# Optimization experiments

Hardware: AMD Instinct MI355X
Metric: run time of the kernel (lower is better)

Reference implementation:

```python
import jax, jax.numpy as jnp
import numpy as np
from jax.scipy.special import logsumexp

EPS_OT = 0.05      # self.eps in AttentionOT
MAX_ITER = 100     # Sinkhorn max_iter (torch early-stops; at convergence results match)


def _l2norm(x):
    # F.normalize(x, dim=-1, p=2) with eps=1e-12
    return x / jnp.maximum(jnp.linalg.norm(x, axis=-1, keepdims=True), 1e-12)


def _sinkhorn(Cmat, mu, nu, eps):
    # Cmat: (BK, M, N), mu: (BK, M), nu: (BK, N)
    log_mu = jnp.log(mu + 1e-8)
    log_nu = jnp.log(nu + 1e-8)

    def kern(u, v):
        # log Boltzmann kernel: (-C + u_i + v_j) / eps, shape (BK, M, N)
        return (-Cmat + u[..., :, None] + v[..., None, :]) / eps

    def step(carry, _):
        u, v = carry
        u = eps * (log_mu - logsumexp(kern(u, v), axis=2)) + u
        v = eps * (log_nu - logsumexp(kern(u, v), axis=1)) + v
        return (u, v), None

    u0 = jnp.zeros_like(mu)
    v0 = jnp.zeros_like(nu)
    (u, v), _ = jax.lax.scan(jax.checkpoint(step), (u0, v0), None, length=MAX_ITER)
    return jnp.exp(kern(u, v))  # transport plan T, (BK, M, N)


def setup_inputs() -> dict:
    key = jax.random.key(0)
    Nq, M, B, K, C = 64, 16, 8, 256, 512
    ks = jax.random.split(key, 8)
    s = 1.0 / np.sqrt(C)  # torch nn.Linear default init bound
    return {
        "xq": jax.random.normal(ks[0], (Nq, M, B, C), jnp.float32),
        "xk": jax.random.normal(ks[1], (B, K, C), jnp.float32),
        "xv": jax.random.normal(ks[2], (B, K, C), jnp.float32),
        "Wq": jax.random.uniform(ks[3], (C, C), jnp.float32, -s, s),
        "Wk": jax.random.uniform(ks[4], (C, C), jnp.float32, -s, s),
        "Wv": jax.random.uniform(ks[5], (C, C), jnp.float32, -s, s),
        "Wp": jax.random.uniform(ks[6], (C, C), jnp.float32, -s, s),
        "bp": jax.random.uniform(ks[7], (C,), jnp.float32, -s, s),
    }


def reference(xq, xk, xv, Wq, Wk, Wv, Wp, bp):
    Nq, M, B, C = xq.shape
    K = xk.shape[1]
    # projections (qkv_bias=False; proj has bias). dropout probs are 0 -> identity.
    q = _l2norm(xq @ Wq.T)          # (Nq, M, B, C)
    kk = _l2norm(xk @ Wk.T)         # (B, K, C)
    v = xv @ Wv.T                   # (B, K, C)
    # torch: einsum('bkc,nmbc->bnkm') then permute(0,2,3,1) -> (B,K,M,Nq)
    sim = jnp.einsum('bkc,nmbc->bkmn', kk, q).reshape(B * K, M, Nq)
    wdist = 1.0 - sim
    mu = jnp.full((B * K, M), 1.0 / M, dtype=sim.dtype)
    nu = jnp.full((B * K, Nq), 1.0 / Nq, dtype=sim.dtype)
    T = _sinkhorn(wdist, mu, nu, EPS_OT)            # (B*K, M, Nq)
    score_map = (M * Nq * sim * T).reshape(B, K, M, Nq)
    attn = T.reshape(B, K, M, Nq).transpose(3, 0, 1, 2)  # (Nq, B, K, M)
    x = jnp.einsum('nbkm,bkc->nmbc', attn, v)            # (Nq, M, B, C)
    x = x @ Wp.T + bp
    return x, score_map
```

## Files before the change

### kernel.cpp

```cpp
#include <hip/hip_runtime.h>


typedef short   short8  __attribute__((ext_vector_type(8)));
typedef float   floatx4 __attribute__((ext_vector_type(4)));
typedef unsigned int uint2e __attribute__((ext_vector_type(2)));

static __device__ __forceinline__ float fastrcp(float x) {
    return __builtin_amdgcn_rcpf(x);
}
static __device__ __forceinline__ unsigned short f2bf(float f) {
    union { float f; unsigned u; } c; c.f = f;
    unsigned r = c.u + 0x7FFF + ((c.u >> 16) & 1);
    return (unsigned short)(r >> 16);
}
static __device__ __forceinline__ float bf2f(unsigned short h) {
    union { unsigned u; float f; } c; c.u = (unsigned)h << 16;
    return c.f;
}

#if __has_builtin(__builtin_amdgcn_permlane16_swap)
static __device__ __forceinline__ float xadd16(float s) {
    uint2e r = __builtin_amdgcn_permlane16_swap(
        __float_as_uint(s), __float_as_uint(s), false, false);
    return __uint_as_float(r.x) + __uint_as_float(r.y);
}
#else
static __device__ __forceinline__ float xadd16(float s) {
    return s + __shfl_xor(s, 16, 64);
}
#endif
#if __has_builtin(__builtin_amdgcn_permlane32_swap)
static __device__ __forceinline__ float xadd32(float s) {
    uint2e r = __builtin_amdgcn_permlane32_swap(
        __float_as_uint(s), __float_as_uint(s), false, false);
    return __uint_as_float(r.x) + __uint_as_float(r.y);
}
#else
static __device__ __forceinline__ float xadd32(float s) {
    return s + __shfl_xor(s, 32, 64);
}
#endif

#define RRI(x, C) __builtin_amdgcn_update_dpp(0, (x), (C), 0xf, 0xf, true)
#define RRF(x, C) __int_as_float(RRI(__float_as_int(x), (C)))
#define GATH16(d, s) do { d[0] = (s);                                        \
    d[1]  = RRF((s), 0x121); d[2]  = RRF((s), 0x122);                        \
    d[3]  = RRF((s), 0x123); d[4]  = RRF((s), 0x124);                        \
    d[5]  = RRF((s), 0x125); d[6]  = RRF((s), 0x126);                        \
    d[7]  = RRF((s), 0x127); d[8]  = RRF((s), 0x128);                        \
    d[9]  = RRF((s), 0x129); d[10] = RRF((s), 0x12a);                        \
    d[11] = RRF((s), 0x12b); d[12] = RRF((s), 0x12c);                        \
    d[13] = RRF((s), 0x12d); d[14] = RRF((s), 0x12e);                        \
    d[15] = RRF((s), 0x12f); } while (0)

__global__ __launch_bounds__(256) void prep(
    const float* __restrict__ xq, const float* __restrict__ xk,
    const float* __restrict__ xv, const float* __restrict__ Wq,
    const float* __restrict__ Wk, const float* __restrict__ Wv,
    const float* __restrict__ Wp,
    unsigned short* __restrict__ xqh, unsigned short* __restrict__ xql,
    unsigned short* __restrict__ xkh, unsigned short* __restrict__ xkl,
    unsigned short* __restrict__ xvb,
    unsigned short* __restrict__ wqh, unsigned short* __restrict__ wql,
    unsigned short* __restrict__ wkh, unsigned short* __restrict__ wkl,
    unsigned short* __restrict__ wvb, unsigned short* __restrict__ wpb)
{
    const int b = blockIdx.x;
    const float* src; unsigned short *dh, *dl; long base;
    if (b < 4096)      { src = xq; dh = xqh; dl = xql;     base = (long)b * 256; }
    else if (b < 5120) { src = xk; dh = xkh; dl = xkl;     base = (long)(b - 4096) * 256; }
    else if (b < 6144) { src = xv; dh = xvb; dl = nullptr; base = (long)(b - 5120) * 256; }
    else if (b < 6400) { src = Wq; dh = wqh; dl = wql;     base = (long)(b - 6144) * 256; }
    else if (b < 6656) { src = Wk; dh = wkh; dl = wkl;     base = (long)(b - 6400) * 256; }
    else if (b < 6912) { src = Wv; dh = wvb; dl = nullptr; base = (long)(b - 6656) * 256; }
    else               { src = Wp; dh = wpb; dl = nullptr; base = (long)(b - 6912) * 256; }
    const long i = base + threadIdx.x;
    float4 v = ((const float4*)src)[i];
    ushort4 h;
    h.x = f2bf(v.x); h.y = f2bf(v.y); h.z = f2bf(v.z); h.w = f2bf(v.w);
    ((ushort4*)dh)[i] = h;
    if (dl) {
        ushort4 l;
        l.x = f2bf(v.x - bf2f(h.x)); l.y = f2bf(v.y - bf2f(h.y));
        l.z = f2bf(v.z - bf2f(h.z)); l.w = f2bf(v.w - bf2f(h.w));
        ((ushort4*)dl)[i] = l;
    }
}

__global__ __launch_bounds__(256, 3) void gemm_qkv2(
    const unsigned short* __restrict__ xqh, const unsigned short* __restrict__ xql,
    const unsigned short* __restrict__ xkh, const unsigned short* __restrict__ xkl,
    const unsigned short* __restrict__ xvb,
    const unsigned short* __restrict__ wqh, const unsigned short* __restrict__ wql,
    const unsigned short* __restrict__ wkh, const unsigned short* __restrict__ wkl,
    const unsigned short* __restrict__ wvb,
    unsigned short* __restrict__ qh, unsigned short* __restrict__ ql,
    unsigned short* __restrict__ kh, unsigned short* __restrict__ kl,
    unsigned short* __restrict__ vt)
{
    __shared__ __align__(16) short LB[15360];
    short (*Ash)[40] = (short(*)[40])(LB);
    short (*Asl)[40] = (short(*)[40])(LB + 2560);
    short (*Bsh)[40] = (short(*)[40])(LB + 5120);
    short (*Bsl)[40] = (short(*)[40])(LB + 10240);

    const int bt = blockIdx.y;
    const unsigned short *Ah, *Al, *Bh, *Bl;
    int seg, arow0;
    if (bt < 128)      { Ah = xqh; Al = xql; Bh = wqh; Bl = wql; arow0 = bt * 64;         seg = 0; }
    else if (bt < 160) { Ah = xkh; Al = xkl; Bh = wkh; Bl = wkl; arow0 = (bt - 128) * 64; seg = 1; }
    else               { Ah = xvb; Al = xvb; Bh = wvb; Bl = wvb; arow0 = (bt - 160) * 64; seg = 2; }
    const bool split = (seg != 2);

    const int tid  = threadIdx.x;
    const int lane = tid & 63, wv = tid >> 6;
    const int wc = wv * 32;
    const int j0 = blockIdx.x * 128;

    floatx4 acc[4][2];
#pragma unroll
    for (int i = 0; i < 4; i++)
#pragma unroll
        for (int j = 0; j < 2; j++) acc[i][j] = {0.f, 0.f, 0.f, 0.f};

    const int sr = tid >> 2, sch = (tid & 3) * 8;
    const int fr = lane & 15, fq = (lane >> 4) * 8;

    for (int k0 = 0; k0 < 512; k0 += 32) {
        {
            const long ao = (long)(arow0 + sr) * 512 + k0 + sch;
            *(short8*)&Ash[sr][sch] = *(const short8*)(Ah + ao);
            if (split) *(short8*)&Asl[sr][sch] = *(const short8*)(Al + ao);
        }
#pragma unroll
        for (int p = 0; p < 2; p++) {
            const int r = sr + p * 64;
            const long bo = (long)(j0 + r) * 512 + k0 + sch;
            *(short8*)&Bsh[r][sch] = *(const short8*)(Bh + bo);
            if (split) *(short8*)&Bsl[r][sch] = *(const short8*)(Bl + bo);
        }
        __syncthreads();
        short8 ah[4], bh[2];
#pragma unroll
        for (int i = 0; i < 4; i++) ah[i] = *(const short8*)&Ash[i * 16 + fr][fq];
#pragma unroll
        for (int j = 0; j < 2; j++) bh[j] = *(const short8*)&Bsh[wc + j * 16 + fr][fq];
        if (split) {
            short8 al[4], bl[2];
#pragma unroll
            for (int i = 0; i < 4; i++) al[i] = *(const short8*)&Asl[i * 16 + fr][fq];
#pragma unroll
            for (int j = 0; j < 2; j++) bl[j] = *(const short8*)&Bsl[wc + j * 16 + fr][fq];
#pragma unroll
            for (int i = 0; i < 4; i++)
#pragma unroll
                for (int j = 0; j < 2; j++) {
                    acc[i][j] = __builtin_amdgcn_mfma_f32_16x16x32_bf16(ah[i], bh[j], acc[i][j], 0, 0, 0);
                    acc[i][j] = __builtin_amdgcn_mfma_f32_16x16x32_bf16(ah[i], bl[j], acc[i][j], 0, 0, 0);
                    acc[i][j] = __builtin_amdgcn_mfma_f32_16x16x32_bf16(al[i], bh[j], acc[i][j], 0, 0, 0);
                }
        } else {
#pragma unroll
            for (int i = 0; i < 4; i++)
#pragma unroll
                for (int j = 0; j < 2; j++)
                    acc[i][j] = __builtin_amdgcn_mfma_f32_16x16x32_bf16(ah[i], bh[j], acc[i][j], 0, 0, 0);
        }
        __syncthreads();
    }

    const int cr = (lane >> 4) * 4, cc = lane & 15;
    if (seg == 2) {
        short (*S2)[72] = (short(*)[72])LB;
#pragma unroll
        for (int i = 0; i < 4; i++)
#pragma unroll
            for (int j = 0; j < 2; j++)
#pragma unroll
                for (int r = 0; r < 4; r++)
                    S2[wc + j * 16 + cc][i * 16 + cr + r] =
                        (short)f2bf(acc[i][j][r]);
        __syncthreads();
        const int orow = tid >> 1;
        const int os   = (tid & 1) * 32;
        unsigned short* dst = vt + (long)(arow0 >> 8) * 131072
                            + (long)(j0 + orow) * 256 + (arow0 & 255) + os;
#pragma unroll
        for (int c8 = 0; c8 < 4; c8++)
            *(short8*)(dst + c8 * 8) = *(const short8*)&S2[orow][os + c8 * 8];
    } else {
#pragma unroll
        for (int i = 0; i < 4; i++)
#pragma unroll
            for (int j = 0; j < 2; j++) {
                const int gj = j0 + wc + j * 16 + cc;
#pragma unroll
                for (int r = 0; r < 4; r++) {
                    const int gi = arow0 + i * 16 + cr + r;
                    const float v = acc[i][j][r];
                    const unsigned short h = f2bf(v);
                    const unsigned short lo = f2bf(v - bf2f(h));
                    if (seg == 0) {
                        const long orow = (long)((gi & 7) * 1024 + ((gi >> 3) & 15) * 64 + (gi >> 7));
                        qh[orow * 512 + gj] = h;
                        ql[orow * 512 + gj] = lo;
                    } else {
                        kh[(long)gi * 512 + gj] = h;
                        kl[(long)gi * 512 + gj] = lo;
                    }
                }
            }
    }
}

__global__ __launch_bounds__(256) void gemm_sim64(
    const short* __restrict__ Ah, const short* __restrict__ Al,
    const short* __restrict__ Bh, const short* __restrict__ Bl,
    float* __restrict__ Out, const float* __restrict__ rs)
{
    const int z = blockIdx.z;
    Ah += (long)z * 131072;  Al += (long)z * 131072;
    Bh += (long)z * 524288;  Bl += (long)z * 524288;
    Out += (long)z * 262144;
    const float* rsq = rs + (long)z * 1024;
    const float* rsk = rs + 8192 + (long)z * 256;

    __shared__ __align__(16) short Ash[64][40];
    __shared__ __align__(16) short Asl[64][40];
    __shared__ __align__(16) short Bsh[64][40];
    __shared__ __align__(16) short Bsl[64][40];

    const int tid  = threadIdx.x;
    const int lane = tid & 63, wv = tid >> 6;
    const int wr = (wv >> 1) * 32, wc = (wv & 1) * 32;
    const int i0 = blockIdx.x * 64, j0 = blockIdx.y * 64;

    floatx4 acc[2][2];
#pragma unroll
    for (int i = 0; i < 2; i++)
#pragma unroll
        for (int j = 0; j < 2; j++) acc[i][j] = {0.f, 0.f, 0.f, 0.f};

    const int sr = tid >> 2, sch = (tid & 3) * 8;
    const int fr = lane & 15, fq = (lane >> 4) * 8;

    for (int k0 = 0; k0 < 512; k0 += 32) {
        const long ao = (long)(i0 + sr) * 512 + k0 + sch;
        const long bo = (long)(j0 + sr) * 512 + k0 + sch;
        *(short8*)&Ash[sr][sch] = *(const short8*)(Ah + ao);
        *(short8*)&Asl[sr][sch] = *(const short8*)(Al + ao);
        *(short8*)&Bsh[sr][sch] = *(const short8*)(Bh + bo);
        *(short8*)&Bsl[sr][sch] = *(const short8*)(Bl + bo);
        __syncthreads();
        short8 ah[2], al[2], bh[2], bl[2];
#pragma unroll
        for (int i = 0; i < 2; i++) {
            ah[i] = *(const short8*)&Ash[wr + i * 16 + fr][fq];
            al[i] = *(const short8*)&Asl[wr + i * 16 + fr][fq];
        }
#pragma unroll
        for (int j = 0; j < 2; j++) {
            bh[j] = *(const short8*)&Bsh[wc + j * 16 + fr][fq];
            bl[j] = *(const short8*)&Bsl[wc + j * 16 + fr][fq];
        }
#pragma unroll
        for (int i = 0; i < 2; i++)
#pragma unroll
            for (int j = 0; j < 2; j++) {
                acc[i][j] = __builtin_amdgcn_mfma_f32_16x16x32_bf16(ah[i], bh[j], acc[i][j], 0, 0, 0);
                acc[i][j] = __builtin_amdgcn_mfma_f32_16x16x32_bf16(ah[i], bl[j], acc[i][j], 0, 0, 0);
                acc[i][j] = __builtin_amdgcn_mfma_f32_16x16x32_bf16(al[i], bh[j], acc[i][j], 0, 0, 0);
            }
        __syncthreads();
    }

    const int cr = (lane >> 4) * 4, cc = lane & 15;
#pragma unroll
    for (int i = 0; i < 2; i++)
#pragma unroll
        for (int j = 0; j < 2; j++) {
            const int gj = j0 + wc + j * 16 + cc;
            const float sq = rsq[gj];
#pragma unroll
            for (int r = 0; r < 4; r++) {
                const int gi = i0 + wr + i * 16 + cr + r;
                Out[(long)gi * 1024 + gj] = acc[i][j][r] * rsk[gi] * sq;
            }
        }
}

template <bool BIAS, bool OPERM, bool OUT_BF16>
__global__ __launch_bounds__(256) void gemm_bf16(
    const short* __restrict__ A, const short* __restrict__ B,
    const float* __restrict__ bias, void* __restrict__ OutV,
    int Kdim, int lda, int ldb, int ldo, long sA, long sB, long sO)
{
    __shared__ __align__(16) short As[128][40];
    __shared__ __align__(16) short Bs[128][40];

    const int tid  = threadIdx.x;
    const int lane = tid & 63, wv = tid >> 6;
    const int wr = (wv >> 1) * 64, wc = (wv & 1) * 64;
    const int i0 = blockIdx.x * 128, j0 = blockIdx.y * 128;

    floatx4 acc[4][4];
#pragma unroll
    for (int i = 0; i < 4; i++)
#pragma unroll
        for (int j = 0; j < 4; j++) acc[i][j] = {0.f, 0.f, 0.f, 0.f};

    const int sr = tid >> 2, sk = (tid & 3) * 8;
    const int fr = lane & 15, fq = (lane >> 4) * 8;
    const short* pa = A + (long)blockIdx.z * sA;
    const short* pb = B + (long)blockIdx.z * sB;

    for (int k0 = 0; k0 < Kdim; k0 += 32) {
#pragma unroll
        for (int p = 0; p < 2; p++) {
            *(short8*)&As[sr + p * 64][sk] =
                *(const short8*)(pa + (long)(i0 + sr + p * 64) * lda + k0 + sk);
            *(short8*)&Bs[sr + p * 64][sk] =
                *(const short8*)(pb + (long)(j0 + sr + p * 64) * ldb + k0 + sk);
        }
        __syncthreads();
        short8 af[4], bf[4];
#pragma unroll
        for (int i = 0; i < 4; i++) af[i] = *(const short8*)&As[wr + i * 16 + fr][fq];
#pragma unroll
        for (int j = 0; j < 4; j++) bf[j] = *(const short8*)&Bs[wc + j * 16 + fr][fq];
#pragma unroll
        for (int i = 0; i < 4; i++)
#pragma unroll
            for (int j = 0; j < 4; j++)
                acc[i][j] = __builtin_amdgcn_mfma_f32_16x16x32_bf16(af[i], bf[j], acc[i][j], 0, 0, 0);
        __syncthreads();
    }

    float* Of = nullptr; unsigned short* Ob = nullptr;
    if constexpr (OUT_BF16) Ob = (unsigned short*)OutV + (long)blockIdx.z * sO;
    else                    Of = (float*)OutV + (long)blockIdx.z * sO;
    const int cr = (lane >> 4) * 4, cc = lane & 15;
#pragma unroll
    for (int i = 0; i < 4; i++) {
#pragma unroll
        for (int j = 0; j < 4; j++) {
            const int gj = j0 + wc + j * 16 + cc;
            float bb = 0.0f;
            if constexpr (BIAS) bb = bias[gj];
#pragma unroll
            for (int r = 0; r < 4; r++) {
                const int gi = i0 + wr + i * 16 + cr + r;
                float v = acc[i][j][r] + bb;
                long idx;
                if constexpr (OPERM)
                    idx = (long)((gi & 63) * 128 + ((gi >> 6) & 15) * 8 + (gi >> 10)) * ldo + gj;
                else
                    idx = (long)gi * ldo + gj;
                if constexpr (OUT_BF16) Ob[idx] = f2bf(v);
                else                    Of[idx] = v;
            }
        }
    }
}

__global__ __launch_bounds__(256) void rownorm(
    const unsigned short* __restrict__ qh, const unsigned short* __restrict__ ql,
    const unsigned short* __restrict__ kh, const unsigned short* __restrict__ kl,
    float* __restrict__ rs)
{
    const int row  = blockIdx.x * 4 + (threadIdx.x >> 6);
    const int lane = threadIdx.x & 63;
    const unsigned short *ph, *pl;
    long r;
    if (row < 8192) { ph = qh; pl = ql; r = row; }
    else            { ph = kh; pl = kl; r = row - 8192; }
    const long o = r * 512 + lane * 8;
    ushort4 h0 = *(const ushort4*)(ph + o), h1 = *(const ushort4*)(ph + o + 4);
    ushort4 l0 = *(const ushort4*)(pl + o), l1 = *(const ushort4*)(pl + o + 4);
    float ss = 0.0f;
    const unsigned short hv[8] = {h0.x, h0.y, h0.z, h0.w, h1.x, h1.y, h1.z, h1.w};
    const unsigned short lv[8] = {l0.x, l0.y, l0.z, l0.w, l1.x, l1.y, l1.z, l1.w};
#pragma unroll
    for (int i = 0; i < 8; i++) {
        const float v = bf2f(hv[i]) + bf2f(lv[i]);
        ss = fmaf(v, v, ss);
    }
#pragma unroll
    for (int off = 32; off; off >>= 1) ss += __shfl_xor(ss, off, 64);
    if (lane == 0) rs[row] = 1.0f / fmaxf(sqrtf(ss), 1e-12f);
}

__global__ __launch_bounds__(256, 2) void sinkhorn5(
    const float* __restrict__ sim, float* __restrict__ score,
    unsigned short* __restrict__ Tt)
{
    const int lane = threadIdx.x & 63;
    const int bk   = blockIdx.x * 4 + (threadIdx.x >> 6);
    const float* S = sim + (long)bk * 1024;
    const int m = lane & 15, g = lane >> 4;

    int idx[16];
    idx[0] = m;
    idx[1]  = RRI(m, 0x121); idx[2]  = RRI(m, 0x122); idx[3]  = RRI(m, 0x123);
    idx[4]  = RRI(m, 0x124); idx[5]  = RRI(m, 0x125); idx[6]  = RRI(m, 0x126);
    idx[7]  = RRI(m, 0x127); idx[8]  = RRI(m, 0x128); idx[9]  = RRI(m, 0x129);
    idx[10] = RRI(m, 0x12a); idx[11] = RRI(m, 0x12b); idx[12] = RRI(m, 0x12c);
    idx[13] = RRI(m, 0x12d); idx[14] = RRI(m, 0x12e); idx[15] = RRI(m, 0x12f);

    float K1[16], K2R[16], sv[16];
#pragma unroll
    for (int j = 0; j < 16; j++) {
        K1[j] = __expf((S[m * 64 + g * 16 + idx[j]] - 1.0f) * 20.0f);
        const float s_ = S[idx[j] * 64 + lane];
        sv[j]  = s_;
        K2R[j] = __expf((s_ - 1.0f) * 20.0f);
    }

    const float muP = 0.0625f + 1e-8f;
    const float nuP = 0.015625f + 1e-8f;
    float b = 1.0f;
    float aB[16], bB[16];
#pragma unroll
    for (int j = 0; j < 16; j++) bB[j] = 1.0f;

#pragma unroll 1
    for (int it = 0; it < 100; it++) {
        float s0 = 0, s1 = 0, s2 = 0, s3 = 0;
#pragma unroll
        for (int j = 0; j < 4; j++) {
            s0 = fmaf(K1[j],      bB[j],      s0);
            s1 = fmaf(K1[4 + j],  bB[4 + j],  s1);
            s2 = fmaf(K1[8 + j],  bB[8 + j],  s2);
            s3 = fmaf(K1[12 + j], bB[12 + j], s3);
        }
        float s = (s0 + s1) + (s2 + s3);
        s = xadd16(s);
        s = xadd32(s);
        const float a = muP * fastrcp(s);
        GATH16(aB, a);
        float t0 = 0, t1 = 0, t2 = 0, t3 = 0;
#pragma unroll
        for (int j = 0; j < 4; j++) {
            t0 = fmaf(K2R[j],      aB[j],      t0);
            t1 = fmaf(K2R[4 + j],  aB[4 + j],  t1);
            t2 = fmaf(K2R[8 + j],  aB[8 + j],  t2);
            t3 = fmaf(K2R[12 + j], aB[12 + j], t3);
        }
        const float bp_ = b;
        b = nuP * fastrcp((t0 + t1) + (t2 + t3));
        GATH16(bB, b);
        const int conv = __builtin_fabsf(b - bp_) <= 1e-5f * __builtin_fabsf(b);
        if (__all(conv)) break;
    }

    float* Sc = score + (long)bk * 1024;
    unsigned short* Tp = Tt + (long)(bk >> 8) * 262144 + (bk & 255);
#pragma unroll
    for (int j = 0; j < 16; j++) {
        const int row = idx[j];
        const float Tv = aB[j] * K2R[j] * b;
        Sc[row * 64 + lane] = 1024.0f * sv[j] * Tv;
        Tp[(long)(row * 64 + lane) * 256] = f2bf(Tv);
    }
}

extern "C" void kernel_launch(void* const* d_in, const int* in_sizes, int n_in,
                              void* d_out, int out_size, void* d_ws, size_t ws_size,
                              hipStream_t stream)
{
    (void)in_sizes; (void)n_in; (void)out_size; (void)ws_size;
    const float* xq = (const float*)d_in[0];
    const float* xk = (const float*)d_in[1];
    const float* xv = (const float*)d_in[2];
    const float* Wq = (const float*)d_in[3];
    const float* Wk = (const float*)d_in[4];
    const float* Wv = (const float*)d_in[5];
    const float* Wp = (const float*)d_in[6];
    const float* bp = (const float*)d_in[7];

    float* out_x     = (float*)d_out;
    float* out_score = out_x + 8192L * 512;

    char* W = (char*)d_ws;
    const long MB = 1 << 20;
    unsigned short* qh   = (unsigned short*)(W + 0);
    unsigned short* ql   = (unsigned short*)(W + 8 * MB);
    unsigned short* xq_h = (unsigned short*)(W + 16 * MB);
    float*          simb = (float*)(W + 16 * MB);
    unsigned short* xq_l = (unsigned short*)(W + 24 * MB);
    unsigned short* xpre = (unsigned short*)(W + 24 * MB);
    unsigned short* xk_h = (unsigned short*)(W + 32 * MB);
    unsigned short* xk_l = (unsigned short*)(W + 34 * MB);
    unsigned short* Tt   = (unsigned short*)(W + 32 * MB);
    unsigned short* xv_b = (unsigned short*)(W + 36 * MB);
    unsigned short* kh   = (unsigned short*)(W + 38 * MB);
    unsigned short* kl   = (unsigned short*)(W + 40 * MB);
    unsigned short* vt   = (unsigned short*)(W + 42 * MB);
    unsigned short* wqh  = (unsigned short*)(W + 44 * MB);
    unsigned short* wql  = (unsigned short*)(W + 44 * MB + 1 * 524288);
    unsigned short* wkh  = (unsigned short*)(W + 44 * MB + 2 * 524288);
    unsigned short* wkl  = (unsigned short*)(W + 44 * MB + 3 * 524288);
    unsigned short* wvb  = (unsigned short*)(W + 44 * MB + 4 * 524288);
    unsigned short* wpb  = (unsigned short*)(W + 44 * MB + 5 * 524288);
    float*          rs   = (float*)(W + 47 * MB);

    const dim3 blk(256);

    prep<<<7168, blk, 0, stream>>>(xq, xk, xv, Wq, Wk, Wv, Wp,
                                   xq_h, xq_l, xk_h, xk_l, xv_b,
                                   wqh, wql, wkh, wkl, wvb, wpb);

    gemm_qkv2<<<dim3(4, 192), blk, 0, stream>>>(
        xq_h, xq_l, xk_h, xk_l, xv_b, wqh, wql, wkh, wkl, wvb,
        qh, ql, kh, kl, vt);

    rownorm<<<2560, blk, 0, stream>>>(qh, ql, kh, kl, rs);

    gemm_sim64<<<dim3(4, 16, 8), blk, 0, stream>>>(
        (const short*)kh, (const short*)kl, (const short*)qh, (const short*)ql,
        simb, rs);

    sinkhorn5<<<512, blk, 0, stream>>>(simb, out_score, Tt);

    gemm_bf16<false, false, true><<<dim3(8, 4, 8), blk, 0, stream>>>(
        (const short*)Tt, (const short*)vt, nullptr, xpre,
        256, 256, 256, 512, 262144, 131072, 524288);

    gemm_bf16<true, true, false><<<dim3(64, 4), blk, 0, stream>>>(
        (const short*)xpre, (const short*)wpb, bp, out_x,
        512, 512, 512, 512, 0, 0, 0);
}
```

Baseline: 200.1 us.

## Double-buffer QKV GEMM with direct-to-LDS loads and fuse row norms into sim GEMM

The QKV projection GEMM now loads tiles with global_load_lds straight into a double-buffered LDS area, prefetching the next K-slice while the current one runs on MFMA. Its grid is transposed so consecutive blocks share the same weight column tile. The separate rownorm kernel is removed; gemm_sim64 now accumulates the squared norms of its q and k rows from the tiles it already loads and applies the normalisation in its epilogue. This drops one launch and a reread of q and k, at the cost of more LDS in the QKV kernel, which may lower its occupancy, and a few extra FMAs per element in the sim GEMM.

```diff
diff --git a/kernel.cpp b/kernel.cpp
--- a/kernel.cpp
+++ b/kernel.cpp
@@ -16,6 +16,12 @@
 static __device__ __forceinline__ float bf2f(unsigned short h) {
     union { unsigned u; float f; } c; c.u = (unsigned)h << 16;
     return c.f;
+}
+
+static __device__ __forceinline__ void gll16(const unsigned short* g, short* l) {
+    __builtin_amdgcn_global_load_lds(
+        (const __attribute__((address_space(1))) void*)g,
+        (__attribute__((address_space(3))) void*)l, 16, 0, 0);
 }
 
 #if __has_builtin(__builtin_amdgcn_permlane16_swap)
@@ -98,13 +104,9 @@
     unsigned short* __restrict__ kh, unsigned short* __restrict__ kl,
     unsigned short* __restrict__ vt)
 {
-    __shared__ __align__(16) short LB[15360];
-    short (*Ash)[40] = (short(*)[40])(LB);
-    short (*Asl)[40] = (short(*)[40])(LB + 2560);
-    short (*Bsh)[40] = (short(*)[40])(LB + 5120);
-    short (*Bsl)[40] = (short(*)[40])(LB + 10240);
-
-    const int bt = blockIdx.y;
+    __shared__ __align__(16) short LB[24576];
+
+    const int bt = blockIdx.x;
     const unsigned short *Ah, *Al, *Bh, *Bl;
     int seg, arow0;
     if (bt < 128)      { Ah = xqh; Al = xql; Bh = wqh; Bl = wql; arow0 = bt * 64;         seg = 0; }
@@ -115,7 +117,7 @@
     const int tid  = threadIdx.x;
     const int lane = tid & 63, wv = tid >> 6;
     const int wc = wv * 32;
-    const int j0 = blockIdx.x * 128;
+    const int j0 = blockIdx.y * 128;
 
     floatx4 acc[4][2];
 #pragma unroll
@@ -123,34 +125,50 @@
 #pragma unroll
         for (int j = 0; j < 2; j++) acc[i][j] = {0.f, 0.f, 0.f, 0.f};
 
-    const int sr = tid >> 2, sch = (tid & 3) * 8;
+    const int lrow = lane >> 2;
+    const int lch  = (lane & 3) * 8;
+    const int gra  = 16 * wv;
+    const int grb  = 32 * wv;
+    const long gA0 = (long)(arow0 + gra + lrow) * 512 + lch;
+    const long gB0 = (long)(j0    + grb + lrow) * 512 + lch;
+
     const int fr = lane & 15, fq = (lane >> 4) * 8;
 
-    for (int k0 = 0; k0 < 512; k0 += 32) {
-        {
-            const long ao = (long)(arow0 + sr) * 512 + k0 + sch;
-            *(short8*)&Ash[sr][sch] = *(const short8*)(Ah + ao);
-            if (split) *(short8*)&Asl[sr][sch] = *(const short8*)(Al + ao);
-        }
-#pragma unroll
-        for (int p = 0; p < 2; p++) {
-            const int r = sr + p * 64;
-            const long bo = (long)(j0 + r) * 512 + k0 + sch;
-            *(short8*)&Bsh[r][sch] = *(const short8*)(Bh + bo);
-            if (split) *(short8*)&Bsl[r][sch] = *(const short8*)(Bl + bo);
-        }
-        __syncthreads();
+#define QKV_STAGE(d, k0) do {                                                 \
+        short* bb = LB + (d) * 12288;                                         \
+        gll16(Ah + gA0 + (k0),            bb + gra * 32);                     \
+        gll16(Bh + gB0 + (k0),            bb + 4096 + grb * 32);              \
+        gll16(Bh + gB0 + (k0) + 16 * 512, bb + 4096 + (grb + 16) * 32);       \
+        if (split) {                                                          \
+            gll16(Al + gA0 + (k0),            bb + 2048 + gra * 32);          \
+            gll16(Bl + gB0 + (k0),            bb + 8192 + grb * 32);          \
+            gll16(Bl + gB0 + (k0) + 16 * 512, bb + 8192 + (grb + 16) * 32);   \
+        }                                                                     \
+    } while (0)
+
+    QKV_STAGE(0, 0);
+    __syncthreads();
+
+#pragma unroll 2
+    for (int t = 0; t < 16; t++) {
+        const int cur = t & 1;
+        if (t < 15) QKV_STAGE(cur ^ 1, (t + 1) * 32);
+        const short* base = LB + cur * 12288;
         short8 ah[4], bh[2];
 #pragma unroll
-        for (int i = 0; i < 4; i++) ah[i] = *(const short8*)&Ash[i * 16 + fr][fq];
-#pragma unroll
-        for (int j = 0; j < 2; j++) bh[j] = *(const short8*)&Bsh[wc + j * 16 + fr][fq];
+        for (int i = 0; i < 4; i++)
+            ah[i] = *(const short8*)&base[(i * 16 + fr) * 32 + fq];
+#pragma unroll
+        for (int j = 0; j < 2; j++)
+            bh[j] = *(const short8*)&base[4096 + (wc + j * 16 + fr) * 32 + fq];
         if (split) {
             short8 al[4], bl[2];
 #pragma unroll
-            for (int i = 0; i < 4; i++) al[i] = *(const short8*)&Asl[i * 16 + fr][fq];
-#pragma unroll
-            for (int j = 0; j < 2; j++) bl[j] = *(const short8*)&Bsl[wc + j * 16 + fr][fq];
+            for (int i = 0; i < 4; i++)
+                al[i] = *(const short8*)&base[2048 + (i * 16 + fr) * 32 + fq];
+#pragma unroll
+            for (int j = 0; j < 2; j++)
+                bl[j] = *(const short8*)&base[8192 + (wc + j * 16 + fr) * 32 + fq];
 #pragma unroll
             for (int i = 0; i < 4; i++)
 #pragma unroll
@@ -168,6 +186,7 @@
         }
         __syncthreads();
     }
+#undef QKV_STAGE
 
     const int cr = (lane >> 4) * 4, cc = lane & 15;
     if (seg == 2) {
@@ -216,19 +235,19 @@
 __global__ __launch_bounds__(256) void gemm_sim64(
     const short* __restrict__ Ah, const short* __restrict__ Al,
     const short* __restrict__ Bh, const short* __restrict__ Bl,
-    float* __restrict__ Out, const float* __restrict__ rs)
+    float* __restrict__ Out)
 {
     const int z = blockIdx.z;
     Ah += (long)z * 131072;  Al += (long)z * 131072;
     Bh += (long)z * 524288;  Bl += (long)z * 524288;
     Out += (long)z * 262144;
-    const float* rsq = rs + (long)z * 1024;
-    const float* rsk = rs + 8192 + (long)z * 256;
 
     __shared__ __align__(16) short Ash[64][40];
     __shared__ __align__(16) short Asl[64][40];
     __shared__ __align__(16) short Bsh[64][40];
     __shared__ __align__(16) short Bsl[64][40];
+    __shared__ float sRA[64];
+    __shared__ float sRB[64];
 
     const int tid  = threadIdx.x;
     const int lane = tid & 63, wv = tid >> 6;
@@ -244,13 +263,26 @@
     const int sr = tid >> 2, sch = (tid & 3) * 8;
     const int fr = lane & 15, fq = (lane >> 4) * 8;
 
+    float ssqA = 0.0f, ssqB = 0.0f;
+
     for (int k0 = 0; k0 < 512; k0 += 32) {
         const long ao = (long)(i0 + sr) * 512 + k0 + sch;
         const long bo = (long)(j0 + sr) * 512 + k0 + sch;
-        *(short8*)&Ash[sr][sch] = *(const short8*)(Ah + ao);
-        *(short8*)&Asl[sr][sch] = *(const short8*)(Al + ao);
-        *(short8*)&Bsh[sr][sch] = *(const short8*)(Bh + bo);
-        *(short8*)&Bsl[sr][sch] = *(const short8*)(Bl + bo);
+        const short8 vah = *(const short8*)(Ah + ao);
+        const short8 val_ = *(const short8*)(Al + ao);
+        const short8 vbh = *(const short8*)(Bh + bo);
+        const short8 vbl = *(const short8*)(Bl + bo);
+        *(short8*)&Ash[sr][sch] = vah;
+        *(short8*)&Asl[sr][sch] = val_;
+        *(short8*)&Bsh[sr][sch] = vbh;
+        *(short8*)&Bsl[sr][sch] = vbl;
+#pragma unroll
+        for (int e = 0; e < 8; e++) {
+            const float va = bf2f((unsigned short)vah[e]) + bf2f((unsigned short)val_[e]);
+            const float vb = bf2f((unsigned short)vbh[e]) + bf2f((unsigned short)vbl[e]);
+            ssqA = fmaf(va, va, ssqA);
+            ssqB = fmaf(vb, vb, ssqB);
+        }
         __syncthreads();
         short8 ah[2], al[2], bh[2], bl[2];
 #pragma unroll
@@ -274,17 +306,26 @@
         __syncthreads();
     }
 
+    ssqA += __shfl_xor(ssqA, 1, 64);  ssqA += __shfl_xor(ssqA, 2, 64);
+    ssqB += __shfl_xor(ssqB, 1, 64);  ssqB += __shfl_xor(ssqB, 2, 64);
+    if ((tid & 3) == 0) {
+        sRA[sr] = 1.0f / fmaxf(sqrtf(ssqA), 1e-12f);
+        sRB[sr] = 1.0f / fmaxf(sqrtf(ssqB), 1e-12f);
+    }
+    __syncthreads();
+
     const int cr = (lane >> 4) * 4, cc = lane & 15;
 #pragma unroll
     for (int i = 0; i < 2; i++)
 #pragma unroll
         for (int j = 0; j < 2; j++) {
-            const int gj = j0 + wc + j * 16 + cc;
-            const float sq = rsq[gj];
+            const int lc = wc + j * 16 + cc;
+            const float sq = sRB[lc];
+            const int gj = j0 + lc;
 #pragma unroll
             for (int r = 0; r < 4; r++) {
-                const int gi = i0 + wr + i * 16 + cr + r;
-                Out[(long)gi * 1024 + gj] = acc[i][j][r] * rsk[gi] * sq;
+                const int lr = wr + i * 16 + cr + r;
+                Out[(long)(i0 + lr) * 1024 + gj] = acc[i][j][r] * sRA[lr] * sq;
             }
         }
 }
@@ -361,33 +402,6 @@
             }
         }
     }
-}
-
-__global__ __launch_bounds__(256) void rownorm(
-    const unsigned short* __restrict__ qh, const unsigned short* __restrict__ ql,
-    const unsigned short* __restrict__ kh, const unsigned short* __restrict__ kl,
-    float* __restrict__ rs)
-{
-    const int row  = blockIdx.x * 4 + (threadIdx.x >> 6);
-    const int lane = threadIdx.x & 63;
-    const unsigned short *ph, *pl;
-    long r;
-    if (row < 8192) { ph = qh; pl = ql; r = row; }
-    else            { ph = kh; pl = kl; r = row - 8192; }
-    const long o = r * 512 + lane * 8;
-    ushort4 h0 = *(const ushort4*)(ph + o), h1 = *(const ushort4*)(ph + o + 4);
-    ushort4 l0 = *(const ushort4*)(pl + o), l1 = *(const ushort4*)(pl + o + 4);
-    float ss = 0.0f;
-    const unsigned short hv[8] = {h0.x, h0.y, h0.z, h0.w, h1.x, h1.y, h1.z, h1.w};
-    const unsigned short lv[8] = {l0.x, l0.y, l0.z, l0.w, l1.x, l1.y, l1.z, l1.w};
-#pragma unroll
-    for (int i = 0; i < 8; i++) {
-        const float v = bf2f(hv[i]) + bf2f(lv[i]);
-        ss = fmaf(v, v, ss);
-    }
-#pragma unroll
-    for (int off = 32; off; off >>= 1) ss += __shfl_xor(ss, off, 64);
-    if (lane == 0) rs[row] = 1.0f / fmaxf(sqrtf(ss), 1e-12f);
 }
 
 __global__ __launch_bounds__(256, 2) void sinkhorn5(
@@ -502,7 +516,6 @@
     unsigned short* wkl  = (unsigned short*)(W + 44 * MB + 3 * 524288);
     unsigned short* wvb  = (unsigned short*)(W + 44 * MB + 4 * 524288);
     unsigned short* wpb  = (unsigned short*)(W + 44 * MB + 5 * 524288);
-    float*          rs   = (float*)(W + 47 * MB);
 
     const dim3 blk(256);
 
@@ -510,15 +523,13 @@
                                    xq_h, xq_l, xk_h, xk_l, xv_b,
                                    wqh, wql, wkh, wkl, wvb, wpb);
 
-    gemm_qkv2<<<dim3(4, 192), blk, 0, stream>>>(
+    gemm_qkv2<<<dim3(192, 4), blk, 0, stream>>>(
         xq_h, xq_l, xk_h, xk_l, xv_b, wqh, wql, wkh, wkl, wvb,
         qh, ql, kh, kl, vt);
 
-    rownorm<<<2560, blk, 0, stream>>>(qh, ql, kh, kl, rs);
-
     gemm_sim64<<<dim3(4, 16, 8), blk, 0, stream>>>(
         (const short*)kh, (const short*)kl, (const short*)qh, (const short*)ql,
-        simb, rs);
+        simb);
 
     sinkhorn5<<<512, blk, 0, stream>>>(simb, out_score, Tt);
 
```

After: 186.8 us. 6.6% less time.
